# Kernel optimization log

Measured on AMD Instinct MI355X. Metric: run time of the kernel, lower is better.

## Reference

```python
import jax, jax.numpy as jnp
import numpy as np

DIM = 768      # model dim
NH = 12        # num heads
WS = 32        # window/input size (H = W = WS)
B = 8          # batch


def _relative_position_index(ws):
    # Mirrors the torch buffer construction.
    coords = np.stack(np.meshgrid(np.arange(ws), np.arange(ws), indexing='ij'))  # [2, ws, ws]
    cf = coords.reshape(2, -1)                                # [2, N]
    rel = cf[:, :, None] - cf[:, None, :]                     # [2, N, N]
    rel = rel.transpose(1, 2, 0).astype(np.int64)             # [N, N, 2]
    rel[..., 0] += ws - 1
    rel[..., 1] += ws - 1
    rel[..., 0] *= 2 * ws - 1
    return rel.sum(-1)                                        # [N, N]


def setup_inputs() -> dict:
    key = jax.random.key(0)
    ks = jax.random.split(key, 5)
    std = 0.02
    x = jax.random.normal(ks[0], (B, WS, WS, DIM), jnp.float32)
    qkv_w = jax.random.normal(ks[1], (3 * DIM, DIM), jnp.float32) * std
    q_bias = jnp.zeros((DIM,), jnp.float32)
    v_bias = jnp.zeros((DIM,), jnp.float32)
    proj_w = jax.random.normal(ks[2], (DIM, DIM), jnp.float32) * std
    proj_b = jnp.zeros((DIM,), jnp.float32)
    num_rel = (2 * WS - 1) * (2 * WS - 1) + 3
    rel_table = jax.random.normal(ks[3], (num_rel, NH), jnp.float32) * std
    rel_index = jnp.asarray(_relative_position_index(WS), jnp.int32)
    return {
        'x': x, 'qkv_w': qkv_w, 'q_bias': q_bias, 'v_bias': v_bias,
        'proj_w': proj_w, 'proj_b': proj_b, 'rel_table': rel_table,
        'rel_index': rel_index,
    }


def reference(x, qkv_w, q_bias, v_bias, proj_w, proj_b, rel_table, rel_index):
    Bb, H, W, C = x.shape
    N = H * W
    hd = C // NH
    scale = hd ** (-0.5)
    # qkv bias: [q_bias, zeros(k), v_bias]
    qkv_b = jnp.concatenate([q_bias, jnp.zeros_like(v_bias), v_bias])
    qkv = x.reshape(Bb, N, C) @ qkv_w.T + qkv_b                # [B, N, 3C]
    qkv = qkv.reshape(Bb, N, 3, NH, hd).transpose(2, 0, 3, 1, 4)  # [3, B, nh, N, hd]
    q, k, v = qkv[0] * scale, qkv[1], qkv[2]
    attn = jnp.einsum('bhqd,bhkd->bhqk', q, k)                 # [B, nh, N, N]
    bias = rel_table[rel_index.reshape(-1)].reshape(N, N, NH)  # [N, N, nh]
    bias = bias.transpose(2, 0, 1)                             # [nh, N, N]
    attn = jax.nn.softmax(attn + bias[None], axis=-1)
    out = jnp.einsum('bhqk,bhkd->bhqd', attn, v)               # [B, nh, N, hd]
    out = out.transpose(0, 2, 1, 3).reshape(Bb, H, W, C)
    return out @ proj_w.T + proj_b
```

## Files before the change

### kernel.cpp

```cpp
#include <hip/hip_runtime.h>
#include <cstdint>
#include <cstddef>

#define DIMC 768
#define NHH  12
#define NSEQ 1024
#define HD   64

#define SX  6291456
#define SW1 1769472
#define SW2 589824

#define RELN 3969
#define RELP 4032

#define NCAST ((SX + SW1 + SW2) / 2048)
#define NRELB ((NHH * RELN + 255) / 256)

#define LOG2E 1.4426950408889634f

typedef _Float16 f16x8 __attribute__((ext_vector_type(8)));
typedef _Float16 f16x4 __attribute__((ext_vector_type(4)));
typedef __fp16   h16x2 __attribute__((ext_vector_type(2)));
typedef float    f32x4 __attribute__((ext_vector_type(4)));
typedef float    f32x16 __attribute__((ext_vector_type(16)));

__device__ inline void gld16(const void* g, void* l) {
  __builtin_amdgcn_global_load_lds(
      (const __attribute__((address_space(1))) void*)g,
      (__attribute__((address_space(3))) void*)l, 16, 0, 0);
}

__global__ __launch_bounds__(256) void cast_f16(
    const float* __restrict__ x, const float* __restrict__ w1,
    const float* __restrict__ w2, _Float16* __restrict__ dst,
    const float* __restrict__ rel_table, float* __restrict__ relT) {
  if (blockIdx.x >= NCAST) {
    const int g = (blockIdx.x - NCAST) * 256 + threadIdx.x;
    if (g < NHH * RELN) {
      const int h = g / RELN, idx = g - h * RELN;
      relT[h * RELP + idx] = rel_table[idx * NHH + h] * LOG2E;
    }
    return;
  }
  const long long t = (long long)blockIdx.x * 256 + threadIdx.x;
  const long long i = t * 8;
  const float* src; long long off;
  if (i < SX) { src = x; off = i; }
  else if (i < SX + SW1) { src = w1; off = i - SX; }
  else { src = w2; off = i - (SX + SW1); }
  const float4 a = *(const float4*)(src + off);
  const float4 b = *(const float4*)(src + off + 4);
  f16x8 o;
  o[0] = (_Float16)a.x; o[1] = (_Float16)a.y; o[2] = (_Float16)a.z; o[3] = (_Float16)a.w;
  o[4] = (_Float16)b.x; o[5] = (_Float16)b.y; o[6] = (_Float16)b.z; o[7] = (_Float16)b.w;
  *(f16x8*)(dst + i) = o;
}

template <int EPI>
__global__ __launch_bounds__(256) void gemm_mfma(
    const _Float16* __restrict__ A, const _Float16* __restrict__ W,
    const float* __restrict__ b0, const float* __restrict__ b1,
    float* __restrict__ outF, _Float16* __restrict__ oq,
    _Float16* __restrict__ ok, _Float16* __restrict__ ovt) {
  __shared__ _Float16 Alds[128 * 64];
  __shared__ _Float16 Blds[64 * 64];

  const int tid = threadIdx.x;
  const int w = tid >> 6, lane = tid & 63, quad = lane >> 4, l16 = lane & 15;
  const int m0 = (blockIdx.x & 63) << 7;
  const int o0 = (blockIdx.x >> 6) << 6;
  const int wr = w * 32;
  const int rkey = l16 & 7;

  f32x4 acc[2][4];
#pragma unroll
  for (int i = 0; i < 2; i++)
#pragma unroll
    for (int j = 0; j < 4; j++) acc[i][j] = (f32x4){0.f, 0.f, 0.f, 0.f};

  const int srow = tid >> 3;
  const int sch = ((tid & 7) ^ (srow & 7)) * 8;
  const _Float16* Ap = A + (size_t)(m0 + srow) * DIMC + sch;
  const _Float16* Wp = W + (size_t)(o0 + srow) * DIMC + sch;
  _Float16* Adst = &Alds[tid * 8];
  _Float16* Bdst = &Blds[tid * 8];

  for (int k0 = 0; k0 < DIMC; k0 += 64) {
    __syncthreads();
#pragma unroll
    for (int k = 0; k < 4; k++)
      gld16(Ap + k0 + k * 32 * DIMC, Adst + k * 2048);
#pragma unroll
    for (int k = 0; k < 2; k++)
      gld16(Wp + k0 + k * 32 * DIMC, Bdst + k * 2048);
    __syncthreads();

#pragma unroll
    for (int ks = 0; ks < 2; ks++) {
      const int ch = (((ks << 2) + quad) ^ rkey) * 8;
      f16x8 a[2], b[4];
#pragma unroll
      for (int i = 0; i < 2; i++)
        a[i] = *(const f16x8*)&Alds[(wr + i * 16 + l16) * 64 + ch];
#pragma unroll
      for (int j = 0; j < 4; j++)
        b[j] = *(const f16x8*)&Blds[(j * 16 + l16) * 64 + ch];
#pragma unroll
      for (int i = 0; i < 2; i++)
#pragma unroll
        for (int j = 0; j < 4; j++)
          acc[i][j] = __builtin_amdgcn_mfma_f32_16x16x32_f16(a[i], b[j], acc[i][j], 0, 0, 0);
    }
  }

  if constexpr (EPI == 0) {
#pragma unroll
    for (int j = 0; j < 4; j++) {
      const int o = o0 + j * 16 + l16;
      const int part = o / DIMC;
      const int cc = o - part * DIMC;
      const int hh = cc >> 6, d = cc & 63;
      const float badd = (part == 0) ? b0[cc] : (part == 2 ? b1[cc] : 0.f);
      if (part == 2) {
#pragma unroll
        for (int i = 0; i < 2; i++) {
          const int mb = m0 + wr + i * 16 + quad * 4;
          const int bb = mb >> 10, n0 = mb & 1023;
          f16x4 vv;
#pragma unroll
          for (int r = 0; r < 4; r++) vv[r] = (_Float16)(acc[i][j][r] + badd);
          *(f16x4*)(ovt + (((size_t)(bb * NHH + hh)) * HD + d) * NSEQ + n0) = vv;
        }
      } else {
        _Float16* dst = (part == 0) ? oq : ok;
#pragma unroll
        for (int i = 0; i < 2; i++) {
#pragma unroll
          for (int r = 0; r < 4; r++) {
            const int m = m0 + wr + i * 16 + quad * 4 + r;
            const int bb = m >> 10, n = m & 1023;
            float v = acc[i][j][r];
            if (part == 0) v = (v + badd) * (0.125f * LOG2E);
            dst[(((size_t)(bb * NHH + hh)) * NSEQ + n) * HD + d] = (_Float16)v;
          }
        }
      }
    }
  } else {
#pragma unroll
    for (int j = 0; j < 4; j++) {
      const int o = o0 + j * 16 + l16;
      const float bo = b0[o];
#pragma unroll
      for (int i = 0; i < 2; i++) {
#pragma unroll
        for (int r = 0; r < 4; r++) {
          const int m = m0 + wr + i * 16 + quad * 4 + r;
          outF[(size_t)m * DIMC + o] = acc[i][j][r] + bo;
        }
      }
    }
  }
}

__global__ __launch_bounds__(256, 3) void flash_mfma(
    const _Float16* __restrict__ Qg, const _Float16* __restrict__ Kg,
    const _Float16* __restrict__ Vtg, const float* __restrict__ relT,
    _Float16* __restrict__ AO) {
  const int nblk = blockIdx.x;
  const int bhl = nblk % 96;
  const int qt = nblk / 96;
  const int head = bhl >> 3, b = bhl & 7;
  const int bh = b * NHH + head;
  const int tid = threadIdx.x, w = tid >> 6, lane = tid & 63;
  const int ql = lane & 31;
  const int hf = lane >> 5;

  __shared__ _Float16 Klds[2][64 * 64];
  __shared__ _Float16 Vlds[2][64 * 64];
  __shared__ __attribute__((aligned(16))) float BiasLds[2][320];

  const int qglob = qt * 128 + w * 32 + ql;
  const _Float16* Qrow = Qg + ((size_t)bh * NSEQ + qglob) * HD + hf * 8;
  f16x8 bq[4];
#pragma unroll
  for (int s = 0; s < 4; s++) bq[s] = *(const f16x8*)(Qrow + s * 16);

  f32x16 O0 = {}, O1 = {};
  float psum = 0.f;
  const h16x2 one2 = {(__fp16)1.f, (__fp16)1.f};

  const _Float16* Kbase = Kg + (size_t)bh * NSEQ * HD;
  const _Float16* Vtbase = Vtg + (size_t)bh * HD * NSEQ;

  const float* relTh = relT + (size_t)head * RELP;
  const int idxb = ql + 31 - 4 * hf;

  const int vrow0 = ql, vrow1 = 32 + ql;
  const int vkey0 = (vrow0 ^ (vrow0 >> 3)) & 7;
  const int vkey1 = (vrow1 ^ (vrow1 >> 3)) & 7;

  const int arow0 = ql,      akey0 = (arow0 ^ (arow0 >> 3)) & 7;
  const int arow1 = 32 + ql, akey1 = (arow1 ^ (arow1 >> 3)) & 7;

  int ks0, ks1, vs0, vs1;
  {
    int c = tid;
    int r = c >> 3, cc = c & 7, key = (r ^ (r >> 3)) & 7;
    ks0 = r * HD + (cc ^ key) * 8;
    vs0 = r * NSEQ + (cc ^ key) * 8;
    c = tid + 256;
    r = c >> 3; cc = c & 7; key = (r ^ (r >> 3)) & 7;
    ks1 = r * HD + (cc ^ key) * 8;
    vs1 = r * NSEQ + (cc ^ key) * 8;
  }

  auto stage = [&](int s, int bsel) {
    const _Float16* Ks = Kbase + (size_t)s * 64 * HD;
    const _Float16* Vs = Vtbase + s * 64;
    gld16(Ks + ks0, &Klds[bsel][tid * 8]);
    gld16(Ks + ks1, &Klds[bsel][(tid + 256) * 8]);
    gld16(Vs + vs0, &Vlds[bsel][tid * 8]);
    gld16(Vs + vs1, &Vlds[bsel][(tid + 256) * 8]);
    if (tid < 79) {
      const int dyLo = qt * 4 + 30 - 2 * s;
      gld16(relTh + dyLo * 63 + tid * 4, &BiasLds[bsel][tid * 4]);
    }
  };

#define SOFTMAX(SV, DW)                                           \
  {                                                               \
    _Pragma("unroll") for (int g = 0; g < 4; g++) {               \
      const float p0 = __builtin_amdgcn_exp2f(SV[4 * g + 0]);     \
      const float p1 = __builtin_amdgcn_exp2f(SV[4 * g + 1]);     \
      const float p2 = __builtin_amdgcn_exp2f(SV[4 * g + 2]);     \
      const float p3 = __builtin_amdgcn_exp2f(SV[4 * g + 3]);     \
      const h16x2 h01 = __builtin_amdgcn_cvt_pkrtz(p0, p1);       \
      const h16x2 h23 = __builtin_amdgcn_cvt_pkrtz(p2, p3);       \
      psum = __builtin_amdgcn_fdot2(h01, one2, psum, false);      \
      psum = __builtin_amdgcn_fdot2(h23, one2, psum, false);      \
      union { h16x2 h; unsigned int u; } c0, c1;                  \
      c0.h = h01; c1.h = h23;                                     \
      DW[2 * g] = c0.u; DW[2 * g + 1] = c1.u;                     \
    }                                                             \
  }

#define PVACC(DW, T)                                                          \
  {                                                                           \
    _Pragma("unroll") for (int s2 = 0; s2 < 2; s2++) {                        \
      const unsigned int x0 = hf ? DW[4 * s2 + 0] : DW[4 * s2 + 2];           \
      const unsigned int x1 = hf ? DW[4 * s2 + 1] : DW[4 * s2 + 3];           \
      const unsigned int y0 = (unsigned int)__shfl_xor((int)x0, 32, 64);      \
      const unsigned int y1 = (unsigned int)__shfl_xor((int)x1, 32, 64);      \
      union { unsigned int u[4]; f16x8 v; } bp;                               \
      if (hf == 0) {                                                          \
        bp.u[0] = DW[4 * s2 + 0]; bp.u[1] = DW[4 * s2 + 1];                   \
        bp.u[2] = y0;             bp.u[3] = y1;                               \
      } else {                                                                \
        bp.u[0] = y0;             bp.u[1] = y1;                               \
        bp.u[2] = DW[4 * s2 + 2]; bp.u[3] = DW[4 * s2 + 3];                   \
      }                                                                       \
      const int kchunk = (T) * 4 + s2 * 2 + hf;                               \
      const f16x8 av0 = *(const f16x8*)&Vlds[cur][((vrow0 << 3) | (kchunk ^ vkey0)) * 8]; \
      O0 = __builtin_amdgcn_mfma_f32_32x32x16_f16(av0, bp.v, O0, 0, 0, 0);    \
      const f16x8 av1 = *(const f16x8*)&Vlds[cur][((vrow1 << 3) | (kchunk ^ vkey1)) * 8]; \
      O1 = __builtin_amdgcn_mfma_f32_32x32x16_f16(av1, bp.v, O1, 0, 0, 0);    \
    }                                                                         \
  }

  stage(0, 0);

  int cur = 0;
#pragma unroll 2
  for (int s = 0; s < 16; s++) {
    __syncthreads();
    if (s + 1 < 16) stage(s + 1, cur ^ 1);

    const float* lb0 = &BiasLds[cur][(w + 1) * 63 + idxb];
    const float* lb1 = &BiasLds[cur][w * 63 + idxb];
    f32x16 S0, S1;
#pragma unroll
    for (int g = 0; g < 4; g++) {
      S0[4 * g + 0] = lb0[-8 * g - 0];
      S0[4 * g + 1] = lb0[-8 * g - 1];
      S0[4 * g + 2] = lb0[-8 * g - 2];
      S0[4 * g + 3] = lb0[-8 * g - 3];
      S1[4 * g + 0] = lb1[-8 * g - 0];
      S1[4 * g + 1] = lb1[-8 * g - 1];
      S1[4 * g + 2] = lb1[-8 * g - 2];
      S1[4 * g + 3] = lb1[-8 * g - 3];
    }

    __builtin_amdgcn_s_setprio(1);
#pragma unroll
    for (int ss = 0; ss < 4; ss++) {
      const f16x8 ak = *(const f16x8*)&Klds[cur][((arow0 << 3) | ((ss * 2 + hf) ^ akey0)) * 8];
      S0 = __builtin_amdgcn_mfma_f32_32x32x16_f16(ak, bq[ss], S0, 0, 0, 0);
    }
#pragma unroll
    for (int ss = 0; ss < 4; ss++) {
      const f16x8 ak = *(const f16x8*)&Klds[cur][((arow1 << 3) | ((ss * 2 + hf) ^ akey1)) * 8];
      S1 = __builtin_amdgcn_mfma_f32_32x32x16_f16(ak, bq[ss], S1, 0, 0, 0);
    }
    __builtin_amdgcn_s_setprio(0);

    unsigned int dw0[8], dw1[8];
    SOFTMAX(S0, dw0);
    __builtin_amdgcn_s_setprio(1);
    PVACC(dw0, 0);
    __builtin_amdgcn_s_setprio(0);
    SOFTMAX(S1, dw1);
    __builtin_amdgcn_s_setprio(1);
    PVACC(dw1, 1);
    __builtin_amdgcn_s_setprio(0);

    cur ^= 1;
  }

  psum += __shfl_xor(psum, 32, 64);
  const float inv = 1.f / psum;
  _Float16* aoRow = AO + ((size_t)(b * NSEQ + qglob)) * DIMC + head * HD;
#pragma unroll
  for (int g = 0; g < 4; g++) {
    f16x4 o0, o1;
#pragma unroll
    for (int j = 0; j < 4; j++) {
      o0[j] = (_Float16)(O0[4 * g + j] * inv);
      o1[j] = (_Float16)(O1[4 * g + j] * inv);
    }
    const int d0 = 8 * g + 4 * hf;
    *(f16x4*)(aoRow + d0) = o0;
    *(f16x4*)(aoRow + 32 + d0) = o1;
  }
}

extern "C" void kernel_launch(void* const* d_in, const int* in_sizes, int n_in,
                              void* d_out, int out_size, void* d_ws, size_t ws_size,
                              hipStream_t stream) {
  const float* x        = (const float*)d_in[0];
  const float* qkv_w    = (const float*)d_in[1];
  const float* q_bias   = (const float*)d_in[2];
  const float* v_bias   = (const float*)d_in[3];
  const float* proj_w   = (const float*)d_in[4];
  const float* proj_b   = (const float*)d_in[5];
  const float* rel_tab  = (const float*)d_in[6];
  float* out = (float*)d_out;

  const size_t NTOK = (size_t)8 * NHH * NSEQ * HD;
  _Float16* Xb     = (_Float16*)d_ws;
  _Float16* Wqkvb  = Xb + SX;
  _Float16* Wprojb = Wqkvb + SW1;
  _Float16* Qb     = Wprojb + SW2;
  _Float16* Kb     = Qb + NTOK;
  _Float16* Vt     = Kb + NTOK;
  float*    relT   = (float*)(Vt + NTOK);
  _Float16* AOb    = Xb;

  cast_f16<<<dim3(NCAST + NRELB), 256, 0, stream>>>(x, qkv_w, proj_w, Xb,
                                                    rel_tab, relT);

  gemm_mfma<0><<<dim3(64 * 36), 256, 0, stream>>>(
      Xb, Wqkvb, q_bias, v_bias, nullptr, Qb, Kb, Vt);

  flash_mfma<<<dim3(768), 256, 0, stream>>>(Qb, Kb, Vt, relT, AOb);

  gemm_mfma<1><<<dim3(64 * 12), 256, 0, stream>>>(
      AOb, Wprojb, proj_b, nullptr, out, nullptr, nullptr, nullptr);
}
```

Baseline: 188.7 us.

## Add 128x96-tile QKV GEMM kernel with 32-wide K steps and higher occupancy

Replaces the QKV projection GEMM with a new kernel that uses 128x96 output tiles (1536 blocks instead of 2304) and a K step of 32, with launch bounds requesting 6 blocks per CU. Each wave computes 2x6 MFMA tiles, giving more reuse of the A fragments per LDS load, and the smaller LDS footprint lets more blocks run per CU. The epilogue writes Q (scaled), K, and transposed V as before. The trade-off is twice as many K iterations, each with its own pair of barriers, and more accumulator registers per thread.

```diff
diff --git a/kernel.cpp b/kernel.cpp
--- a/kernel.cpp
+++ b/kernel.cpp
@@ -55,6 +55,91 @@
   o[0] = (_Float16)a.x; o[1] = (_Float16)a.y; o[2] = (_Float16)a.z; o[3] = (_Float16)a.w;
   o[4] = (_Float16)b.x; o[5] = (_Float16)b.y; o[6] = (_Float16)b.z; o[7] = (_Float16)b.w;
   *(f16x8*)(dst + i) = o;
+}
+
+__global__ __launch_bounds__(256, 6) void gemm_qkv96(
+    const _Float16* __restrict__ A, const _Float16* __restrict__ W,
+    const float* __restrict__ b0, const float* __restrict__ b1,
+    _Float16* __restrict__ oq, _Float16* __restrict__ ok,
+    _Float16* __restrict__ ovt) {
+  __shared__ _Float16 Alds[128 * 32];
+  __shared__ _Float16 Blds[96 * 32];
+
+  const int tid = threadIdx.x;
+  const int w = tid >> 6, lane = tid & 63, quad = lane >> 4, l16 = lane & 15;
+  const int m0 = (blockIdx.x & 63) << 7;
+  const int o0 = (blockIdx.x >> 6) * 96;
+  const int wr = w * 32;
+  const int rkey = (l16 >> 1) & 3;
+
+  f32x4 acc[2][6];
+#pragma unroll
+  for (int i = 0; i < 2; i++)
+#pragma unroll
+    for (int j = 0; j < 6; j++) acc[i][j] = (f32x4){0.f, 0.f, 0.f, 0.f};
+
+  const int r0 = tid >> 2;
+  const int scol = ((tid & 3) ^ ((tid >> 3) & 3)) * 8;
+  const _Float16* Ap0 = A + (size_t)(m0 + r0) * DIMC + scol;
+  const _Float16* Ap1 = Ap0 + (size_t)64 * DIMC;
+  const _Float16* Wp0 = W + (size_t)(o0 + r0) * DIMC + scol;
+  const _Float16* Wp1 = Wp0 + (size_t)64 * DIMC;
+
+  for (int k0 = 0; k0 < DIMC; k0 += 32) {
+    __syncthreads();
+    gld16(Ap0 + k0, &Alds[tid * 8]);
+    gld16(Ap1 + k0, &Alds[(tid + 256) * 8]);
+    gld16(Wp0 + k0, &Blds[tid * 8]);
+    if (tid < 128) gld16(Wp1 + k0, &Blds[(tid + 256) * 8]);
+    __syncthreads();
+
+    const int ch = (quad ^ rkey) * 8;
+    f16x8 a[2], b[6];
+#pragma unroll
+    for (int i = 0; i < 2; i++)
+      a[i] = *(const f16x8*)&Alds[(wr + i * 16 + l16) * 32 + ch];
+#pragma unroll
+    for (int j = 0; j < 6; j++)
+      b[j] = *(const f16x8*)&Blds[(j * 16 + l16) * 32 + ch];
+#pragma unroll
+    for (int i = 0; i < 2; i++)
+#pragma unroll
+      for (int j = 0; j < 6; j++)
+        acc[i][j] = __builtin_amdgcn_mfma_f32_16x16x32_f16(a[i], b[j], acc[i][j], 0, 0, 0);
+  }
+
+#pragma unroll
+  for (int j = 0; j < 6; j++) {
+    const int o = o0 + j * 16 + l16;
+    const int part = o / DIMC;
+    const int cc = o - part * DIMC;
+    const int hh = cc >> 6, d = cc & 63;
+    const float badd = (part == 0) ? b0[cc] : (part == 2 ? b1[cc] : 0.f);
+    if (part == 2) {
+#pragma unroll
+      for (int i = 0; i < 2; i++) {
+        const int mb = m0 + wr + i * 16 + quad * 4;
+        const int bb = mb >> 10, n0 = mb & 1023;
+        f16x4 vv;
+#pragma unroll
+        for (int r = 0; r < 4; r++) vv[r] = (_Float16)(acc[i][j][r] + badd);
+        *(f16x4*)(ovt + (((size_t)(bb * NHH + hh)) * HD + d) * NSEQ + n0) = vv;
+      }
+    } else {
+      _Float16* dst = (part == 0) ? oq : ok;
+#pragma unroll
+      for (int i = 0; i < 2; i++) {
+#pragma unroll
+        for (int r = 0; r < 4; r++) {
+          const int m = m0 + wr + i * 16 + quad * 4 + r;
+          const int bb = m >> 10, n = m & 1023;
+          float v = acc[i][j][r];
+          if (part == 0) v = (v + badd) * (0.125f * LOG2E);
+          dst[(((size_t)(bb * NHH + hh)) * NSEQ + n) * HD + d] = (_Float16)v;
+        }
+      }
+    }
+  }
 }
 
 template <int EPI>
@@ -360,8 +445,8 @@
   cast_f16<<<dim3(NCAST + NRELB), 256, 0, stream>>>(x, qkv_w, proj_w, Xb,
                                                     rel_tab, relT);
 
-  gemm_mfma<0><<<dim3(64 * 36), 256, 0, stream>>>(
-      Xb, Wqkvb, q_bias, v_bias, nullptr, Qb, Kb, Vt);
+  gemm_qkv96<<<dim3(64 * 24), 256, 0, stream>>>(
+      Xb, Wqkvb, q_bias, v_bias, Qb, Kb, Vt);
 
   flash_mfma<<<dim3(768), 256, 0, stream>>>(Qb, Kb, Vt, relT, AOb);
 
```

Measured after the change: 252.3 us. +33.7%, slower.
